# Optimization experiments

Measured on AMD Instinct MI355X. Metric: run time of the kernel, lower is better.

## Reference

```python
import jax, jax.numpy as jnp
import numpy as np

B = 32          # batch size
M = 32          # manifold_dim = phase_dim // 2
H = 128         # hidden_dim
EPS = 1e-6


def _init(k, shape, fan_in):
    return jax.random.normal(k, shape, jnp.float32) / np.sqrt(fan_in)


def setup_inputs() -> dict:
    key = jax.random.key(0)
    ks = jax.random.split(key, 12)
    return {
        "points": jax.random.normal(ks[0], (B, M), jnp.float32),
        # metric_network: M -> H -> M*M (ReLU)
        "Wm1": _init(ks[1], (M, H), M), "bm1": jnp.zeros((H,), jnp.float32),
        "Wm2": _init(ks[2], (H, M * M), H), "bm2": jnp.zeros((M * M,), jnp.float32),
        # christoffel_network: 3 -> H -> 1 (Tanh)
        "Wc1": _init(ks[3], (3, H), 3), "bc1": jnp.zeros((H,), jnp.float32),
        "Wc2": _init(ks[4], (H, 1), H), "bc2": jnp.zeros((1,), jnp.float32),
        # ricci_network: 4M -> 2H -> M*M (ReLU)
        "Wr1": _init(ks[5], (4 * M, 2 * H), 4 * M), "br1": jnp.zeros((2 * H,), jnp.float32),
        "Wr2": _init(ks[6], (2 * H, M * M), 2 * H), "br2": jnp.zeros((M * M,), jnp.float32),
        # flow_network: 2M -> H -> M (ReLU)
        "Wf1": _init(ks[7], (2 * M, H), 2 * M), "bf1": jnp.zeros((H,), jnp.float32),
        "Wf2": _init(ks[8], (H, M), H), "bf2": jnp.zeros((M,), jnp.float32),
        # hamiltonian MLP: 2M -> H -> 2M (Tanh)
        "Wh1": _init(ks[9], (2 * M, H), 2 * M), "bh1": jnp.zeros((H,), jnp.float32),
        "Wh2": _init(ks[10], (H, 2 * M), H), "bh2": jnp.zeros((2 * M,), jnp.float32),
    }


def _geometric_flow(points, Wm1, bm1, Wm2, bm2, Wc1, bc1, Wc2, bc2,
                    Wr1, br1, Wr2, br2, Wf1, bf1, Wf2, bf2, Wh1, bh1, Wh2, bh2):
    b = points.shape[0]
    # --- metric: (b, M, M), symmetrized, eps-regularized ---
    comps = jax.nn.relu(points @ Wm1 + bm1) @ Wm2 + bm2
    metric = comps.reshape(b, M, M) + EPS * jnp.eye(M, dtype=points.dtype)
    metric = 0.5 * (metric + jnp.swapaxes(metric, -1, -2))

    # --- Christoffel: batch over all (i,j,k) triples in one GEMM pass ---
    g_ij = jnp.broadcast_to(metric[:, :, :, None], (b, M, M, M))               # g[i,j]
    g_jk = jnp.broadcast_to(metric[:, None, :, :], (b, M, M, M))               # g[j,k]
    g_ki = jnp.broadcast_to(jnp.swapaxes(metric, 1, 2)[:, :, None, :], (b, M, M, M))  # g[k,i]
    c_in = jnp.stack([g_ij, g_jk, g_ki], axis=-1)                               # (b,M,M,M,3)
    chris = (jnp.tanh(c_in @ Wc1 + bc1) @ Wc2 + bc2)[..., 0]                    # (b,M,M,M)

    # --- Ricci: batch over all (i,j) pairs ---
    pts_b = jnp.broadcast_to(points[:, None, None, :], (b, M, M, M))
    gi = jnp.broadcast_to(metric[:, :, None, :], (b, M, M, M))   # metric[:, i]
    gj = jnp.broadcast_to(metric[:, None, :, :], (b, M, M, M))   # metric[:, j]
    r_in = jnp.concatenate([pts_b, gi, gj, chris], axis=-1)       # (b,M,M,4M)
    r_out = (jax.nn.relu(r_in @ Wr1 + br1) @ Wr2 + br2).reshape(b, M, M, M, M)
    r_out = 0.5 * (r_out + jnp.swapaxes(r_out, -1, -2))
    ricci = r_out.sum(axis=(1, 2)) / (M * M)                      # (b,M,M)

    # --- flow vector ---
    ricci_dir = jnp.einsum('bij,bj->bi', ricci, points)
    f_in = jnp.concatenate([points, ricci_dir], axis=-1)
    flow_vec = jax.nn.relu(f_in @ Wf1 + bf1) @ Wf2 + bf2

    new_pos = points + flow_vec
    phase = jnp.concatenate([new_pos, jnp.zeros_like(points)], axis=-1)  # (b, 2M)

    # --- Hamiltonian evolution (MLP stand-in) ---
    evolved = jnp.tanh(phase @ Wh1 + bh1) @ Wh2 + bh2
    return evolved


def reference(points, Wm1, bm1, Wm2, bm2, Wc1, bc1, Wc2, bc2,
              Wr1, br1, Wr2, br2, Wf1, bf1, Wf2, bf2, Wh1, bh1, Wh2, bh2):
    return _geometric_flow(points, Wm1, bm1, Wm2, bm2, Wc1, bc1, Wc2, bc2,
                           Wr1, br1, Wr2, br2, Wf1, bf1, Wf2, bf2, Wh1, bh1, Wh2, bh2)
```

## Files before the change

### kernel.cpp

```cpp
#include <hip/hip_runtime.h>

#define B 32
#define M 32
#define H 128
#define EPS 1e-6f
#define TSCALE 2.8853900817779268f

typedef float v2f __attribute__((ext_vector_type(2)));
typedef float v4f __attribute__((ext_vector_type(4)));

static __device__ __forceinline__ v2f splat2(float x) { return (v2f){x, x}; }
static __device__ __forceinline__ v4f splat4(float x) { return (v4f){x, x, x, x}; }
static __device__ __forceinline__ v2f fma2(v2f a, v2f b, v2f c) {
    return __builtin_elementwise_fma(a, b, c);
}
static __device__ __forceinline__ v4f fma4(v4f a, v4f b, v4f c) {
    return __builtin_elementwise_fma(a, b, c);
}


#define FMA4(P, s, W) \
    P.x = fmaf((s), (W).x, P.x); P.y = fmaf((s), (W).y, P.y); \
    P.z = fmaf((s), (W).z, P.z); P.w = fmaf((s), (W).w, P.w);

__global__ __launch_bounds__(256) void k_prep(
    const float* __restrict__ points, const float* __restrict__ Wm1,
    const float* __restrict__ bm1, const float* __restrict__ Wm2,
    const float* __restrict__ bm2, const float* __restrict__ Wr1,
    const float* __restrict__ bc1, const float* __restrict__ Wc2,
    const float* __restrict__ bc2, const float* __restrict__ Wr2,
    const float* __restrict__ br2,
    float* __restrict__ metric, float* __restrict__ mj,
    float* __restrict__ S, float* __restrict__ bc1s, float* __restrict__ Kc,
    int* __restrict__ cnt, float* __restrict__ Wp, float* __restrict__ c2)
{
    __shared__ float sbuf[3392];
    const int role = blockIdx.x, t = threadIdx.x;

    if (role >= B) {
        const int u = role - B;
        float* row    = sbuf;
        float* rowsym = sbuf + 1056;
        float* ps     = sbuf + 2208;
        const float* src = (u < 256) ? (Wr2 + u * 1024) : br2;
        #pragma unroll
        for (int r = 0; r < 4; ++r) {
            const int d = t + 256 * r;
            row[(d >> 5) * 33 + (d & 31)] = src[d];
            ps[(d >> 5) * 36 + (d & 31)]  = points[d];
        }
        __syncthreads();
        #pragma unroll
        for (int r = 0; r < 4; ++r) {
            const int d = t + 256 * r, ii = d >> 5, jj = d & 31;
            rowsym[ii * 36 + jj] = 0.5f * (row[ii * 33 + jj] + row[jj * 33 + ii]);
        }
        __syncthreads();
        const int b = t >> 3, i0 = (t & 7) * 4;
        const float4* rs4 = (const float4*)rowsym;
        const float4* p4  = (const float4*)(ps + b * 36);
        float4 o; o.x = o.y = o.z = o.w = 0.f;
        #pragma unroll
        for (int m = 0; m < 8; ++m) {
            const float4 pv = p4[m];
            const float4 r0 = rs4[(i0 + 0) * 9 + m];
            const float4 r1 = rs4[(i0 + 1) * 9 + m];
            const float4 r2 = rs4[(i0 + 2) * 9 + m];
            const float4 r3 = rs4[(i0 + 3) * 9 + m];
            o.x = fmaf(pv.x, r0.x, fmaf(pv.y, r0.y, fmaf(pv.z, r0.z, fmaf(pv.w, r0.w, o.x))));
            o.y = fmaf(pv.x, r1.x, fmaf(pv.y, r1.y, fmaf(pv.z, r1.z, fmaf(pv.w, r1.w, o.y))));
            o.z = fmaf(pv.x, r2.x, fmaf(pv.y, r2.y, fmaf(pv.z, r2.z, fmaf(pv.w, r2.w, o.z))));
            o.w = fmaf(pv.x, r3.x, fmaf(pv.y, r3.y, fmaf(pv.z, r3.z, fmaf(pv.w, r3.w, o.w))));
        }
        if (u < 256) ((float4*)(Wp + u * 1024 + b * 32))[t & 7] = o;
        else         ((float4*)(c2 + b * 32))[t & 7] = o;
        return;
    }

    const int b = role;
    float* p     = sbuf;
    float* h     = sbuf + 32;
    float* comps = sbuf + 160;
    float* msym  = sbuf + 1216;
    if (t < M) p[t] = points[b * M + t];
    __syncthreads();
    if (t < H) {
        float acc = bm1[t];
        #pragma unroll
        for (int m = 0; m < M; ++m) acc = fmaf(p[m], Wm1[m * H + t], acc);
        h[t] = fmaxf(acc, 0.f);
    }
    __syncthreads();
    {
        float4 acc = ((const float4*)bm2)[t];
        const float4* Wm2_4 = (const float4*)Wm2;
        const float4* h4 = (const float4*)h;
        #pragma unroll 2
        for (int u4 = 0; u4 < 32; ++u4) {
            const float4 hv = h4[u4];
            const float4 w0 = Wm2_4[(u4 * 4 + 0) * 256 + t];
            const float4 w1 = Wm2_4[(u4 * 4 + 1) * 256 + t];
            const float4 w2 = Wm2_4[(u4 * 4 + 2) * 256 + t];
            const float4 w3 = Wm2_4[(u4 * 4 + 3) * 256 + t];
            FMA4(acc, hv.x, w0); FMA4(acc, hv.y, w1);
            FMA4(acc, hv.z, w2); FMA4(acc, hv.w, w3);
        }
        const int row = t >> 3, col0 = (t & 7) * 4;
        comps[row * 33 + col0 + 0] = acc.x;
        comps[row * 33 + col0 + 1] = acc.y;
        comps[row * 33 + col0 + 2] = acc.z;
        comps[row * 33 + col0 + 3] = acc.w;
    }
    __syncthreads();
    {
        const int row = t >> 3, col0 = (t & 7) * 4;
        #pragma unroll
        for (int c = 0; c < 4; ++c) {
            const int d = 4 * t + c, ii = row, jj = col0 + c;
            float v = 0.5f * (comps[ii * 33 + jj] + comps[jj * 33 + ii]) + (ii == jj ? EPS : 0.f);
            metric[b * M * M + d] = v;
            msym[d] = v;
        }
    }
    S[b * 256 + t] = 0.f;
    if (t == 0) cnt[b] = 0;
    __syncthreads();
    float wreg[M];
    #pragma unroll
    for (int m = 0; m < M; ++m) wreg[m] = Wr1[(64 + m) * 256 + t];
    const float4* msym4 = (const float4*)msym;
    #pragma unroll 2
    for (int x = 0; x < M; ++x) {
        float acc = 0.f;
        #pragma unroll
        for (int mq = 0; mq < 8; ++mq) {
            float4 mv = msym4[x * 8 + mq];
            acc = fmaf(mv.x, wreg[4 * mq + 0], acc);
            acc = fmaf(mv.y, wreg[4 * mq + 1], acc);
            acc = fmaf(mv.z, wreg[4 * mq + 2], acc);
            acc = fmaf(mv.w, wreg[4 * mq + 3], acc);
        }
        mj[(b * M + x) * 256 + t] = acc;
    }
    if (b == 0) {
        if (t < H) bc1s[t] = bc1[t] * TSCALE;
        if (t == 0) {
            float s = bc2[0];
            for (int u = 0; u < H; ++u) s += Wc2[u];
            Kc[0] = s;
        }
    }
}

__global__ __launch_bounds__(512, 6) void k_main(
    const float* __restrict__ points, const float* __restrict__ metric,
    const float* __restrict__ mj, const float* __restrict__ Wc1,
    const float* __restrict__ Wc2, const float* __restrict__ bc1s,
    const float* __restrict__ Kc, const float* __restrict__ Wr1,
    const float* __restrict__ br1, float* __restrict__ S,
    int* __restrict__ cnt,
    const float* __restrict__ Wp, const float* __restrict__ c2,
    const float* __restrict__ Wf1, const float* __restrict__ bf1,
    const float* __restrict__ Wf2, const float* __restrict__ bf2,
    const float* __restrict__ Wh1, const float* __restrict__ bh1,
    const float* __restrict__ Wh2, const float* __restrict__ bh2,
    float* __restrict__ out)
{
    const int blk = blockIdx.x;
    const int b = blk & 31, i = blk >> 5;
    const int t = threadIdx.x;

    __shared__ float wr1c[M * 256];
    __shared__ float mc[M * M];
    __shared__ float bmi[256];
    __shared__ float Slds[256];
    __shared__ int finflag;

    {
        const float4* src = (const float4*)(Wr1 + 96 * 256);
        float4* dst = (float4*)wr1c;
        #pragma unroll
        for (int r = 0; r < 4; ++r) dst[t + 512 * r] = src[t + 512 * r];
    }
    mc[t] = metric[b * 1024 + t];
    mc[t + 512] = metric[b * 1024 + t + 512];
    if (t < 256) Slds[t] = 0.f;
    __syncthreads();

    if (t < 256) {
        float acc = br1[t];
        #pragma unroll
        for (int m = 0; m < M; ++m) acc = fmaf(points[b * M + m], Wr1[m * 256 + t], acc);
        #pragma unroll
        for (int m = 0; m < M; ++m) acc = fmaf(mc[i * M + m], Wr1[(32 + m) * 256 + t], acc);
        bmi[t] = acc;
    }

    const int w = t >> 6, l = t & 63;
    const int ph = l >> 5, k = l & 31;
    const int j0 = 2 * w + ph, j1 = 16 + 2 * w + ph;
    const float gki  = mc[i * M + k] * TSCALE;
    const v2f gijv = {mc[i * M + j0] * TSCALE, mc[i * M + j1] * TSCALE};
    const v2f gjkv = {mc[j0 * M + k] * TSCALE, mc[j1 * M + k] * TSCALE};
    __syncthreads();

    const v4f* mj4 = (const v4f*)(mj + b * M * 256);
    const int jb = w * 2;
    v4f p00 = mj4[(jb + 0) * 64 + l];
    v4f p01 = mj4[(jb + 1) * 64 + l];
    v4f p10 = mj4[(jb + 16) * 64 + l];
    v4f p11 = mj4[(jb + 17) * 64 + l];

    v2f acc2 = {0.f, 0.f};
    #pragma unroll 8
    for (int u = 0; u < H; ++u) {
        const float tc = fmaf(gki, Wc1[2 * H + u], bc1s[u]);
        v2f pre = fma2(gijv, splat2(Wc1[u]), fma2(gjkv, splat2(Wc1[H + u]), splat2(tc)));
        v2f e = {__builtin_amdgcn_exp2f(pre.x), __builtin_amdgcn_exp2f(pre.y)};
        e += (v2f){1.f, 1.f};
        const v2f r = {__builtin_amdgcn_rcpf(e.x), __builtin_amdgcn_rcpf(e.y)};
        acc2 = fma2(r, splat2(Wc2[u]), acc2);
    }
    const float KcV = Kc[0];
    mc[w * 128 + k * 4 + ph]     = fmaf(-2.f, acc2.x, KcV);
    mc[w * 128 + k * 4 + 2 + ph] = fmaf(-2.f, acc2.y, KcV);

    const v4f* wr1c4 = (const v4f*)wr1c;
    const v4f* ch4 = (const v4f*)(mc + w * 128);
    const v4f bmiv = ((const v4f*)bmi)[l];
    p00 += bmiv; p01 += bmiv; p10 += bmiv; p11 += bmiv;

    #define STEP(W, kk) { \
        const v4f s = ch4[kk]; \
        p00 = fma4(splat4(s.x), W, p00); p01 = fma4(splat4(s.y), W, p01); \
        p10 = fma4(splat4(s.z), W, p10); p11 = fma4(splat4(s.w), W, p11); }

    #pragma unroll
    for (int kc = 0; kc < 4; ++kc) {
        const int kb = kc * 8;
        const v4f w0 = wr1c4[(kb + 0) * 64 + l];
        const v4f w1 = wr1c4[(kb + 1) * 64 + l];
        const v4f w2 = wr1c4[(kb + 2) * 64 + l];
        const v4f w3 = wr1c4[(kb + 3) * 64 + l];
        const v4f w4 = wr1c4[(kb + 4) * 64 + l];
        const v4f w5 = wr1c4[(kb + 5) * 64 + l];
        const v4f w6 = wr1c4[(kb + 6) * 64 + l];
        const v4f w7 = wr1c4[(kb + 7) * 64 + l];
        STEP(w0, kb + 0) STEP(w1, kb + 1) STEP(w2, kb + 2) STEP(w3, kb + 3)
        STEP(w4, kb + 4) STEP(w5, kb + 5) STEP(w6, kb + 6) STEP(w7, kb + 7)
    }
    #undef STEP

    const v4f z4 = {0.f, 0.f, 0.f, 0.f};
    const v4f r00 = __builtin_elementwise_max(p00, z4);
    const v4f r01 = __builtin_elementwise_max(p01, z4);
    const v4f r10 = __builtin_elementwise_max(p10, z4);
    const v4f r11 = __builtin_elementwise_max(p11, z4);
    const v4f rs = (r00 + r01) + (r10 + r11);
    atomicAdd(&Slds[4*l + 0], rs.x);
    atomicAdd(&Slds[4*l + 1], rs.y);
    atomicAdd(&Slds[4*l + 2], rs.z);
    atomicAdd(&Slds[4*l + 3], rs.w);
    __syncthreads();
    if (t < 256) atomicAdd(&S[b * 256 + t], Slds[t]);
    asm volatile("s_waitcnt vmcnt(0)" ::: "memory");
    __syncthreads();
    if (t == 0) {
        int old = atomicAdd(&cnt[b], 1);
        finflag = (old == 31);
    }
    __syncthreads();
    if (!finflag) return;

    float* fs   = wr1c;
    float* rdp  = wr1c + 256;
    float* pl   = wr1c + 768;
    float* fin  = wr1c + 800;
    float* hf   = wr1c + 864;
    float* npos = wr1c + 992;
    float* hh   = wr1c + 1024;

    if (t < 256) fs[t] = atomicAdd(&S[b * 256 + t], 0.f) * (1.f / 1024.f);
    if (t < M) pl[t] = points[b * M + t];
    __syncthreads();
    {
        const int ii = t & 31, ch = t >> 5;
        float part = 0.f;
        #pragma unroll
        for (int uu = 0; uu < 16; ++uu) {
            const int u = ch * 16 + uu;
            part = fmaf(fs[u], Wp[u * 1024 + b * 32 + ii], part);
        }
        rdp[t] = part;
    }
    __syncthreads();
    if (t < M) {
        float a = c2[b * 32 + t];
        #pragma unroll
        for (int ch = 0; ch < 16; ++ch) a += rdp[ch * 32 + t];
        fin[t] = pl[t];
        fin[M + t] = a;
    }
    __syncthreads();
    if (t < H) {
        float acc = bf1[t];
        #pragma unroll
        for (int m = 0; m < 2 * M; ++m) acc = fmaf(fin[m], Wf1[m * H + t], acc);
        hf[t] = fmaxf(acc, 0.f);
    }
    __syncthreads();
    if (t < M) {
        float acc = bf2[t];
        #pragma unroll
        for (int u = 0; u < H; ++u) acc = fmaf(hf[u], Wf2[u * M + t], acc);
        npos[t] = pl[t] + acc;
    }
    __syncthreads();
    if (t < H) {
        float acc = bh1[t];
        #pragma unroll
        for (int m = 0; m < M; ++m) acc = fmaf(npos[m], Wh1[m * H + t], acc);
        hh[t] = tanhf(acc);
    }
    __syncthreads();
    if (t < 2 * M) {
        float acc = bh2[t];
        #pragma unroll
        for (int u = 0; u < H; ++u) acc = fmaf(hh[u], Wh2[u * (2 * M) + t], acc);
        out[b * (2 * M) + t] = acc;
    }
}

extern "C" void kernel_launch(void* const* d_in, const int* in_sizes, int n_in,
                              void* d_out, int out_size, void* d_ws, size_t ws_size,
                              hipStream_t stream)
{
    const float* points = (const float*)d_in[0];
    const float* Wm1 = (const float*)d_in[1];
    const float* bm1 = (const float*)d_in[2];
    const float* Wm2 = (const float*)d_in[3];
    const float* bm2 = (const float*)d_in[4];
    const float* Wc1 = (const float*)d_in[5];
    const float* bc1 = (const float*)d_in[6];
    const float* Wc2 = (const float*)d_in[7];
    const float* bc2 = (const float*)d_in[8];
    const float* Wr1 = (const float*)d_in[9];
    const float* br1 = (const float*)d_in[10];
    const float* Wr2 = (const float*)d_in[11];
    const float* br2 = (const float*)d_in[12];
    const float* Wf1 = (const float*)d_in[13];
    const float* bf1 = (const float*)d_in[14];
    const float* Wf2 = (const float*)d_in[15];
    const float* bf2 = (const float*)d_in[16];
    const float* Wh1 = (const float*)d_in[17];
    const float* bh1 = (const float*)d_in[18];
    const float* Wh2 = (const float*)d_in[19];
    const float* bh2 = (const float*)d_in[20];
    float* out = (float*)d_out;

    float* ws     = (float*)d_ws;
    float* metric = ws;
    float* mj     = ws + 32768;
    float* S      = ws + 294912;
    float* bc1s   = ws + 303104;
    float* Kc     = ws + 303232;
    int*   cnt    = (int*)(ws + 303236);
    float* Wp     = ws + 303268;
    float* c2     = ws + 565412;

    k_prep<<<289, 256, 0, stream>>>(points, Wm1, bm1, Wm2, bm2, Wr1, bc1, Wc2,
                                    bc2, Wr2, br2, metric, mj, S, bc1s, Kc,
                                    cnt, Wp, c2);
    k_main<<<B * M, 512, 0, stream>>>(points, metric, mj, Wc1, Wc2, bc1s, Kc,
                                      Wr1, br1, S, cnt,
                                      Wp, c2, Wf1, bf1, Wf2, bf2,
                                      Wh1, bh1, Wh2, bh2, out);
}
```

Baseline: 60.42 us.

## Precompute per-row bias in prep kernel and overlap Wr1 staging with Christoffel loop

Moves the per-(b,i) Ricci first-layer bias (points and metric row times Wr1 plus br1) out of the main kernel into the prep kernel, which writes it to a new workspace buffer. The main kernel no longer stages the metric into LDS. It reads metric values directly from global memory and loads its Wr1 slice into registers before the Christoffel tanh loop, writing them to LDS only afterwards, so the early barriers are removed and the load latency overlaps with compute. The occupancy hint on k_main is relaxed and the prep kernel does twice the FMA work per block. Register pressure in k_main may rise from holding the staged weights.

Result: no change. 59.37 us (-1.7%).

```diff
diff --git a/kernel.cpp b/kernel.cpp
--- a/kernel.cpp
+++ b/kernel.cpp
@@ -27,12 +27,13 @@
     const float* __restrict__ points, const float* __restrict__ Wm1,
     const float* __restrict__ bm1, const float* __restrict__ Wm2,
     const float* __restrict__ bm2, const float* __restrict__ Wr1,
-    const float* __restrict__ bc1, const float* __restrict__ Wc2,
-    const float* __restrict__ bc2, const float* __restrict__ Wr2,
-    const float* __restrict__ br2,
+    const float* __restrict__ br1, const float* __restrict__ bc1,
+    const float* __restrict__ Wc2, const float* __restrict__ bc2,
+    const float* __restrict__ Wr2, const float* __restrict__ br2,
     float* __restrict__ metric, float* __restrict__ mj,
     float* __restrict__ S, float* __restrict__ bc1s, float* __restrict__ Kc,
-    int* __restrict__ cnt, float* __restrict__ Wp, float* __restrict__ c2)
+    int* __restrict__ cnt, float* __restrict__ Wp, float* __restrict__ c2,
+    float* __restrict__ bmi_pre)
 {
     __shared__ float sbuf[3392];
     const int role = blockIdx.x, t = threadIdx.x;
@@ -125,22 +126,32 @@
     S[b * 256 + t] = 0.f;
     if (t == 0) cnt[b] = 0;
     __syncthreads();
-    float wreg[M];
+    float wreg[M], wreg2[M];
     #pragma unroll
-    for (int m = 0; m < M; ++m) wreg[m] = Wr1[(64 + m) * 256 + t];
+    for (int m = 0; m < M; ++m) {
+        wreg[m]  = Wr1[(64 + m) * 256 + t];
+        wreg2[m] = Wr1[(32 + m) * 256 + t];
+    }
+    float pbr = br1[t];
+    #pragma unroll
+    for (int m = 0; m < M; ++m) pbr = fmaf(p[m], Wr1[m * 256 + t], pbr);
     const float4* msym4 = (const float4*)msym;
-    #pragma unroll 2
     for (int x = 0; x < M; ++x) {
-        float acc = 0.f;
+        float acc = 0.f, acc2 = pbr;
         #pragma unroll
         for (int mq = 0; mq < 8; ++mq) {
             float4 mv = msym4[x * 8 + mq];
-            acc = fmaf(mv.x, wreg[4 * mq + 0], acc);
-            acc = fmaf(mv.y, wreg[4 * mq + 1], acc);
-            acc = fmaf(mv.z, wreg[4 * mq + 2], acc);
-            acc = fmaf(mv.w, wreg[4 * mq + 3], acc);
+            acc  = fmaf(mv.x, wreg[4 * mq + 0], acc);
+            acc  = fmaf(mv.y, wreg[4 * mq + 1], acc);
+            acc  = fmaf(mv.z, wreg[4 * mq + 2], acc);
+            acc  = fmaf(mv.w, wreg[4 * mq + 3], acc);
+            acc2 = fmaf(mv.x, wreg2[4 * mq + 0], acc2);
+            acc2 = fmaf(mv.y, wreg2[4 * mq + 1], acc2);
+            acc2 = fmaf(mv.z, wreg2[4 * mq + 2], acc2);
+            acc2 = fmaf(mv.w, wreg2[4 * mq + 3], acc2);
         }
         mj[(b * M + x) * 256 + t] = acc;
+        bmi_pre[(b * M + x) * 256 + t] = acc2;
     }
     if (b == 0) {
         if (t < H) bc1s[t] = bc1[t] * TSCALE;
@@ -152,12 +163,12 @@
     }
 }
 
-__global__ __launch_bounds__(512, 6) void k_main(
+__global__ __launch_bounds__(512) void k_main(
     const float* __restrict__ points, const float* __restrict__ metric,
-    const float* __restrict__ mj, const float* __restrict__ Wc1,
-    const float* __restrict__ Wc2, const float* __restrict__ bc1s,
-    const float* __restrict__ Kc, const float* __restrict__ Wr1,
-    const float* __restrict__ br1, float* __restrict__ S,
+    const float* __restrict__ mj, const float* __restrict__ bmi_pre,
+    const float* __restrict__ Wc1, const float* __restrict__ Wc2,
+    const float* __restrict__ bc1s, const float* __restrict__ Kc,
+    const float* __restrict__ Wr1, float* __restrict__ S,
     int* __restrict__ cnt,
     const float* __restrict__ Wp, const float* __restrict__ c2,
     const float* __restrict__ Wf1, const float* __restrict__ bf1,
@@ -169,47 +180,33 @@
     const int blk = blockIdx.x;
     const int b = blk & 31, i = blk >> 5;
     const int t = threadIdx.x;
+    const int w = t >> 6, l = t & 63;
+    const int ph = l >> 5, k = l & 31;
 
     __shared__ float wr1c[M * 256];
-    __shared__ float mc[M * M];
-    __shared__ float bmi[256];
+    __shared__ float chlds[8 * 128];
     __shared__ float Slds[256];
     __shared__ int finflag;
 
-    {
-        const float4* src = (const float4*)(Wr1 + 96 * 256);
-        float4* dst = (float4*)wr1c;
-        #pragma unroll
-        for (int r = 0; r < 4; ++r) dst[t + 512 * r] = src[t + 512 * r];
-    }
-    mc[t] = metric[b * 1024 + t];
-    mc[t + 512] = metric[b * 1024 + t + 512];
-    if (t < 256) Slds[t] = 0.f;
-    __syncthreads();
-
-    if (t < 256) {
-        float acc = br1[t];
-        #pragma unroll
-        for (int m = 0; m < M; ++m) acc = fmaf(points[b * M + m], Wr1[m * 256 + t], acc);
-        #pragma unroll
-        for (int m = 0; m < M; ++m) acc = fmaf(mc[i * M + m], Wr1[(32 + m) * 256 + t], acc);
-        bmi[t] = acc;
-    }
-
-    const int w = t >> 6, l = t & 63;
-    const int ph = l >> 5, k = l & 31;
+    const float* mb = metric + b * 1024;
     const int j0 = 2 * w + ph, j1 = 16 + 2 * w + ph;
-    const float gki  = mc[i * M + k] * TSCALE;
-    const v2f gijv = {mc[i * M + j0] * TSCALE, mc[i * M + j1] * TSCALE};
-    const v2f gjkv = {mc[j0 * M + k] * TSCALE, mc[j1 * M + k] * TSCALE};
-    __syncthreads();
-
+    const float gki  = mb[i * M + k] * TSCALE;
+    const v2f gijv = {mb[i * M + j0] * TSCALE, mb[i * M + j1] * TSCALE};
+    const v2f gjkv = {mb[j0 * M + k] * TSCALE, mb[j1 * M + k] * TSCALE};
     const v4f* mj4 = (const v4f*)(mj + b * M * 256);
     const int jb = w * 2;
     v4f p00 = mj4[(jb + 0) * 64 + l];
     v4f p01 = mj4[(jb + 1) * 64 + l];
     v4f p10 = mj4[(jb + 16) * 64 + l];
     v4f p11 = mj4[(jb + 17) * 64 + l];
+    const v4f bmiv = ((const v4f*)(bmi_pre + (b * M + i) * 256))[l];
+    v4f wst0, wst1, wst2, wst3;
+    {
+        const v4f* src = (const v4f*)(Wr1 + 96 * 256);
+        wst0 = src[t];       wst1 = src[t + 512];
+        wst2 = src[t + 1024]; wst3 = src[t + 1536];
+    }
+    if (t < 256) Slds[t] = 0.f;
 
     v2f acc2 = {0.f, 0.f};
     #pragma unroll 8
@@ -222,12 +219,18 @@
         acc2 = fma2(r, splat2(Wc2[u]), acc2);
     }
     const float KcV = Kc[0];
-    mc[w * 128 + k * 4 + ph]     = fmaf(-2.f, acc2.x, KcV);
-    mc[w * 128 + k * 4 + 2 + ph] = fmaf(-2.f, acc2.y, KcV);
+    chlds[w * 128 + k * 4 + ph]     = fmaf(-2.f, acc2.x, KcV);
+    chlds[w * 128 + k * 4 + 2 + ph] = fmaf(-2.f, acc2.y, KcV);
+
+    {
+        v4f* dst = (v4f*)wr1c;
+        dst[t] = wst0;        dst[t + 512] = wst1;
+        dst[t + 1024] = wst2; dst[t + 1536] = wst3;
+    }
+    __syncthreads();
 
     const v4f* wr1c4 = (const v4f*)wr1c;
-    const v4f* ch4 = (const v4f*)(mc + w * 128);
-    const v4f bmiv = ((const v4f*)bmi)[l];
+    const v4f* ch4 = (const v4f*)(chlds + w * 128);
     p00 += bmiv; p01 += bmiv; p10 += bmiv; p11 += bmiv;
 
     #define STEP(W, kk) { \
@@ -358,21 +361,22 @@
     const float* bh2 = (const float*)d_in[20];
     float* out = (float*)d_out;
 
-    float* ws     = (float*)d_ws;
-    float* metric = ws;
-    float* mj     = ws + 32768;
-    float* S      = ws + 294912;
-    float* bc1s   = ws + 303104;
-    float* Kc     = ws + 303232;
-    int*   cnt    = (int*)(ws + 303236);
-    float* Wp     = ws + 303268;
-    float* c2     = ws + 565412;
-
-    k_prep<<<289, 256, 0, stream>>>(points, Wm1, bm1, Wm2, bm2, Wr1, bc1, Wc2,
-                                    bc2, Wr2, br2, metric, mj, S, bc1s, Kc,
-                                    cnt, Wp, c2);
-    k_main<<<B * M, 512, 0, stream>>>(points, metric, mj, Wc1, Wc2, bc1s, Kc,
-                                      Wr1, br1, S, cnt,
+    float* ws      = (float*)d_ws;
+    float* metric  = ws;
+    float* mj      = ws + 32768;
+    float* S       = ws + 294912;
+    float* bc1s    = ws + 303104;
+    float* Kc      = ws + 303232;
+    int*   cnt     = (int*)(ws + 303236);
+    float* Wp      = ws + 303268;
+    float* c2      = ws + 565412;
+    float* bmi_pre = ws + 566436;
+
+    k_prep<<<289, 256, 0, stream>>>(points, Wm1, bm1, Wm2, bm2, Wr1, br1, bc1,
+                                    Wc2, bc2, Wr2, br2, metric, mj, S, bc1s,
+                                    Kc, cnt, Wp, c2, bmi_pre);
+    k_main<<<B * M, 512, 0, stream>>>(points, metric, mj, bmi_pre, Wc1, Wc2,
+                                      bc1s, Kc, Wr1, S, cnt,
                                       Wp, c2, Wf1, bf1, Wf2, bf2,
                                       Wh1, bh1, Wh2, bh2, out);
 }
```
